# Optimization experiments

Measured on AMD Instinct MI355X. Metric: run time of the kernel, lower is better.

Reference implementation:

```python
import jax, jax.numpy as jnp
import numpy as np

B, L, H, E = 4, 2048, 8, 64  # S == L

def setup_inputs() -> dict:
    key = jax.random.key(0)
    k1, k2, k3, k4, k5 = jax.random.split(key, 5)
    q = jax.random.normal(k1, (B, L, H, E), dtype=jnp.float32)
    k = jax.random.normal(k2, (B, L, H, E), dtype=jnp.float32)
    v = jax.random.normal(k3, (B, L, H, E), dtype=jnp.float32)
    tau = jax.random.uniform(k4, (B, 1), dtype=jnp.float32) + 0.5  # positive scale
    delta = jax.random.normal(k5, (B, L), dtype=jnp.float32) * 0.1
    return {"q": q, "k": k, "v": v, "tau": tau, "delta": delta}

def reference(q, k, v, tau, delta):
    # De-stationarized attention: scores = (QK^T) * tau + delta, softmax(scale*scores)
    E_ = q.shape[-1]
    scale = 1.0 / jnp.sqrt(jnp.float32(E_))
    # tau: [B,1] -> [B,1,1,1]; delta: [B,S] -> [B,1,1,S]
    scores = jnp.einsum('blhe,bshe->bhls', q, k) * tau[:, None, None] + delta[:, None, None, :]
    a = jax.nn.softmax(scale * scores, axis=-1)  # dropout is identity in eval / p=0
    out = jnp.einsum('bhls,bshd->blhd', a, v)
    return out, a
```

## Files before the change

kernel.cpp:

```cpp
#include <hip/hip_runtime.h>
#include <stdint.h>

#define B_ 4
#define L_ 2048
#define H_ 8
#define E_ 64
#define S_ 2048

typedef __bf16 bf16x8 __attribute__((ext_vector_type(8)));
typedef _Float16 f16x8 __attribute__((ext_vector_type(8)));
typedef _Float16 f16x4 __attribute__((ext_vector_type(4)));
typedef float f32x4 __attribute__((ext_vector_type(4)));
typedef unsigned short u16;
typedef u16 u16x4 __attribute__((ext_vector_type(4)));

__device__ __forceinline__ u16 f32_to_bf16(float f) {
  union { float f; uint32_t u; } x;
  x.f = f;
  uint32_t u = x.u;
  return (u16)((u + 0x7FFFu + ((u >> 16) & 1u)) >> 16);
}

__global__ __launch_bounds__(256) void prep_qkd(
    const float* __restrict__ q, const float* __restrict__ k,
    const float* __restrict__ tau, const float* __restrict__ delta,
    u16* __restrict__ qb, u16* __restrict__ kb, float* __restrict__ dl) {
  int idx = blockIdx.x * 256 + threadIdx.x;
  int i4 = idx * 4;
  int b = i4 >> 20;
  const float C = 0.125f * 1.44269504088896f;
  float ts = tau[b] * C;
  f32x4 qv = *(const f32x4*)(q + i4);
  f32x4 kv = *(const f32x4*)(k + i4);
  u16x4 qs, ks;
#pragma unroll
  for (int j = 0; j < 4; ++j) {
    qs[j] = f32_to_bf16(qv[j] * ts);
    ks[j] = f32_to_bf16(kv[j]);
  }
  *(u16x4*)(qb + i4) = qs;
  *(u16x4*)(kb + i4) = ks;
  if (idx < (B_ * S_) / 4) {
    f32x4 dv = *(const f32x4*)(delta + i4);
    f32x4 ds = {dv[0] * C, dv[1] * C, dv[2] * C, dv[3] * C};
    *(f32x4*)(dl + i4) = ds;
  }
}

__global__ __launch_bounds__(256) void prep_v(const float* __restrict__ v,
                                              u16* __restrict__ vb) {
  __shared__ float t[32][33];
  int bid = blockIdx.x;
  int et = bid & 1;
  int st = (bid >> 1) & 63;
  int h = (bid >> 7) & 7;
  int b = bid >> 10;
  int tx = threadIdx.x & 31;
  int ty = threadIdx.x >> 5;
#pragma unroll
  for (int k2 = 0; k2 < 4; ++k2) {
    int s = st * 32 + ty + 8 * k2;
    int e = et * 32 + tx;
    t[ty + 8 * k2][tx] = v[(((size_t)b * S_ + s) * H_ + h) * E_ + e];
  }
  __syncthreads();
#pragma unroll
  for (int k2 = 0; k2 < 4; ++k2) {
    int e = et * 32 + ty + 8 * k2;
    int s = st * 32 + tx;
    _Float16 hf = (_Float16)t[tx][ty + 8 * k2];
    vb[(((size_t)b * H_ + h) * E_ + e) * S_ + s] = __builtin_bit_cast(u16, hf);
  }
}

__global__ __launch_bounds__(512, 4) void attn_fused(
    const u16* __restrict__ qb, const u16* __restrict__ kb,
    const u16* __restrict__ vbuf, const float* __restrict__ dl,
    float* __restrict__ out, float* __restrict__ oa) {
  __shared__ __align__(16) u16 sc[16 * 2048];
  __shared__ float psum[8][16];
  __shared__ float ox[4][16][17];

  int bid = blockIdx.x;
  int swz = (bid & 7) * 512 + (bid >> 3);
  int b = swz >> 10;
  int h = (swz >> 7) & 7;
  int qt = swz & 127;
  int m0 = qt * 16;
  int tid = threadIdx.x, lane = tid & 63, wave = tid >> 6;
  int l15 = lane & 15, l4 = lane >> 4;
  int s0 = wave * 256;
  int xm = (l15 & 7) << 4;
  char* scb = (char*)sc;

  const u16* qp = qb + (((size_t)b * L_ + (m0 + l15)) * H_ + h) * E_ + 8 * l4;
  bf16x8 qa0 = *(const bf16x8*)qp;
  bf16x8 qa1 = *(const bf16x8*)(qp + 32);

  const u16* kbase = kb + (((size_t)b * S_ + (s0 + l15)) * H_ + h) * E_ + 8 * l4;
  const float* dbase = dl + b * S_ + s0 + 4 * l4;

  float sums = 0.f;
#pragma unroll 4
  for (int t = 0; t < 16; ++t) {
    const u16* kp = kbase + (size_t)t * (16 * H_ * E_);
    bf16x8 ka0 = *(const bf16x8*)kp;
    bf16x8 ka1 = *(const bf16x8*)(kp + 32);
    f32x4 dv = *(const f32x4*)(dbase + 16 * t);
    f32x4 acc = {0.f, 0.f, 0.f, 0.f};
    acc = __builtin_amdgcn_mfma_f32_16x16x32_bf16(ka0, qa0, acc, 0, 0, 0);
    acc = __builtin_amdgcn_mfma_f32_16x16x32_bf16(ka1, qa1, acc, 0, 0, 0);
    float p0 = __builtin_amdgcn_exp2f(acc[0] + dv[0]);
    float p1 = __builtin_amdgcn_exp2f(acc[1] + dv[1]);
    float p2 = __builtin_amdgcn_exp2f(acc[2] + dv[2]);
    float p3 = __builtin_amdgcn_exp2f(acc[3] + dv[3]);
    sums += (p0 + p1) + (p2 + p3);
    f16x4 pv = {(_Float16)p0, (_Float16)p1, (_Float16)p2, (_Float16)p3};
    int off = (l15 << 12) + (((s0 << 1) + (t << 5) + (l4 << 3)) ^ xm);
    *(f16x4*)(scb + off) = pv;
  }
  sums += __shfl_xor(sums, 16, 64);
  sums += __shfl_xor(sums, 32, 64);
  if (lane < 16) psum[wave][lane] = sums;
  __syncthreads();

  float zq[2];

  {
    int et = wave & 3;
    int h2 = wave >> 2;
    const u16* vb0 =
        vbuf + ((size_t)(b * H_ + h) * E_ + 16 * et + l15) * S_ + h2 * 1024 + 8 * l4;
    const char* sch = scb + (l15 << 12) + (h2 << 11);
    f32x4 oaccA = {0.f, 0.f, 0.f, 0.f};
    f32x4 oaccB = {0.f, 0.f, 0.f, 0.f};
#pragma unroll 4
    for (int c = 0; c < 32; c += 2) {
      f16x8 af0 = *(const f16x8*)(sch + (((c << 6) + (l4 << 4)) ^ xm));
      f16x8 vf0 = *(const f16x8*)(vb0 + (c << 5));
      oaccA = __builtin_amdgcn_mfma_f32_16x16x32_f16(af0, vf0, oaccA, 0, 0, 0);
      f16x8 af1 = *(const f16x8*)(sch + ((((c + 1) << 6) + (l4 << 4)) ^ xm));
      f16x8 vf1 = *(const f16x8*)(vb0 + ((c + 1) << 5));
      oaccB = __builtin_amdgcn_mfma_f32_16x16x32_f16(af1, vf1, oaccB, 0, 0, 0);
    }
    oaccA += oaccB;
    if (h2 == 1) {
#pragma unroll
      for (int r = 0; r < 4; ++r) ox[et][4 * l4 + r][l15] = oaccA[r];
    }
    __syncthreads();
    if (h2 == 0) {
#pragma unroll
      for (int r = 0; r < 4; ++r) {
        int row = 4 * l4 + r;
        float zr = psum[0][row] + psum[1][row] + psum[2][row] + psum[3][row] +
                   psum[4][row] + psum[5][row] + psum[6][row] + psum[7][row];
        float o = oaccA[r] + ox[et][row][l15];
        out[(((size_t)b * L_ + (m0 + row)) * H_ + h) * E_ + 16 * et + l15] =
            o / zr;
      }
    }
  }

  {
    int row = 2 * wave + (lane >> 5);
    int l31 = lane & 31;
    float zrow = psum[0][row] + psum[1][row] + psum[2][row] + psum[3][row] +
                 psum[4][row] + psum[5][row] + psum[6][row] + psum[7][row];
    float zi = 1.f / zrow;
    float* ar = oa + (((size_t)(b * H_ + h)) * L_ + (m0 + row)) * S_;
    int xr = (row & 7) << 4;
    const char* scr = scb + (row << 12);
#pragma unroll 4
    for (int it = 0; it < 8; ++it) {
      f16x8 pv = *(const f16x8*)(scr + (((it << 9) + (l31 << 4)) ^ xr));
      f32x4 lo = {(float)pv[0] * zi, (float)pv[1] * zi,
                  (float)pv[2] * zi, (float)pv[3] * zi};
      f32x4 hi = {(float)pv[4] * zi, (float)pv[5] * zi,
                  (float)pv[6] * zi, (float)pv[7] * zi};
      int col = it * 256 + l31 * 8;
      *(f32x4*)(ar + col) = lo;
      *(f32x4*)(ar + col + 4) = hi;
    }
  }
}

extern "C" void kernel_launch(void* const* d_in, const int* in_sizes, int n_in,
                              void* d_out, int out_size, void* d_ws, size_t ws_size,
                              hipStream_t stream) {
  (void)in_sizes; (void)n_in; (void)out_size;
  const float* q = (const float*)d_in[0];
  const float* k = (const float*)d_in[1];
  const float* v = (const float*)d_in[2];
  const float* tau = (const float*)d_in[3];
  const float* delta = (const float*)d_in[4];
  float* out = (float*)d_out;
  float* oa = out + (size_t)B_ * L_ * H_ * E_;

  const size_t NQ = (size_t)B_ * L_ * H_ * E_;
  u16* qb = (u16*)d_ws;
  u16* kb = qb + NQ;
  u16* vb = kb + NQ;
  float* dl = (float*)(vb + NQ);
  size_t need = 3 * NQ * sizeof(u16) + (size_t)B_ * S_ * sizeof(float);
  if (ws_size < need) return;

  prep_qkd<<<4096, 256, 0, stream>>>(q, k, tau, delta, qb, kb, dl);
  prep_v<<<4096, 256, 0, stream>>>(v, vb);
  attn_fused<<<4096, 512, 0, stream>>>(qb, kb, vb, dl, out, oa);
}
```

Measured before the change: 341.9 us.

## Specialize waves: four compute PV while four stream normalized attention matrix

Splits the eight waves into two roles after the softmax stage. Waves 0-3 compute the P·V product, each doing two MFMAs per shared A fragment across 32 output columns. Waves 4-7 at the same time write the normalized fp32 attention matrix to global memory. This overlaps the large attention-matrix store with the PV compute instead of running them one after the other. The cost is fewer waves issuing stores and an extra barrier before the final output reduction.

```diff
diff --git a/kernel.cpp b/kernel.cpp
--- a/kernel.cpp
+++ b/kernel.cpp
@@ -79,7 +79,7 @@
     float* __restrict__ out, float* __restrict__ oa) {
   __shared__ __align__(16) u16 sc[16 * 2048];
   __shared__ float psum[8][16];
-  __shared__ float ox[4][16][17];
+  __shared__ float ox[2][16][33];
 
   int bid = blockIdx.x;
   int swz = (bid & 7) * 512 + (bid >> 3);
@@ -124,63 +124,66 @@
   if (lane < 16) psum[wave][lane] = sums;
   __syncthreads();
 
-  float zq[2];
-
-  {
-    int et = wave & 3;
-    int h2 = wave >> 2;
-    const u16* vb0 =
-        vbuf + ((size_t)(b * H_ + h) * E_ + 16 * et + l15) * S_ + h2 * 1024 + 8 * l4;
-    const char* sch = scb + (l15 << 12) + (h2 << 11);
-    f32x4 oaccA = {0.f, 0.f, 0.f, 0.f};
-    f32x4 oaccB = {0.f, 0.f, 0.f, 0.f};
+  f32x4 o0 = {0.f, 0.f, 0.f, 0.f};
+  f32x4 o1 = {0.f, 0.f, 0.f, 0.f};
+  int eh = wave & 1;
+
+  if (wave < 4) {
+    int sh = wave >> 1;
+    const u16* vb0 = vbuf + ((size_t)(b * H_ + h) * E_ + 32 * eh + l15) * S_ +
+                     sh * 1024 + 8 * l4;
+    const char* sch = scb + (l15 << 12) + (sh << 11);
 #pragma unroll 4
-    for (int c = 0; c < 32; c += 2) {
-      f16x8 af0 = *(const f16x8*)(sch + (((c << 6) + (l4 << 4)) ^ xm));
-      f16x8 vf0 = *(const f16x8*)(vb0 + (c << 5));
-      oaccA = __builtin_amdgcn_mfma_f32_16x16x32_f16(af0, vf0, oaccA, 0, 0, 0);
-      f16x8 af1 = *(const f16x8*)(sch + ((((c + 1) << 6) + (l4 << 4)) ^ xm));
-      f16x8 vf1 = *(const f16x8*)(vb0 + ((c + 1) << 5));
-      oaccB = __builtin_amdgcn_mfma_f32_16x16x32_f16(af1, vf1, oaccB, 0, 0, 0);
-    }
-    oaccA += oaccB;
-    if (h2 == 1) {
-#pragma unroll
-      for (int r = 0; r < 4; ++r) ox[et][4 * l4 + r][l15] = oaccA[r];
-    }
-    __syncthreads();
-    if (h2 == 0) {
+    for (int c = 0; c < 32; ++c) {
+      f16x8 af = *(const f16x8*)(sch + (((c << 6) + (l4 << 4)) ^ xm));
+      f16x8 v0 = *(const f16x8*)(vb0 + (c << 5));
+      f16x8 v1 = *(const f16x8*)(vb0 + 16 * S_ + (c << 5));
+      o0 = __builtin_amdgcn_mfma_f32_16x16x32_f16(af, v0, o0, 0, 0, 0);
+      o1 = __builtin_amdgcn_mfma_f32_16x16x32_f16(af, v1, o1, 0, 0, 0);
+    }
+    if (sh == 1) {
 #pragma unroll
       for (int r = 0; r < 4; ++r) {
-        int row = 4 * l4 + r;
-        float zr = psum[0][row] + psum[1][row] + psum[2][row] + psum[3][row] +
+        ox[eh][4 * l4 + r][l15] = o0[r];
+        ox[eh][4 * l4 + r][16 + l15] = o1[r];
+      }
+    }
+  } else {
+    int w4 = wave - 4;
+#pragma unroll
+    for (int rr = 0; rr < 4; ++rr) {
+      int row = w4 * 4 + rr;
+      float zrow = psum[0][row] + psum[1][row] + psum[2][row] + psum[3][row] +
                    psum[4][row] + psum[5][row] + psum[6][row] + psum[7][row];
-        float o = oaccA[r] + ox[et][row][l15];
-        out[(((size_t)b * L_ + (m0 + row)) * H_ + h) * E_ + 16 * et + l15] =
-            o / zr;
+      float zi = 1.f / zrow;
+      float* ar = oa + (((size_t)(b * H_ + h)) * L_ + (m0 + row)) * S_;
+      int xr = (row & 7) << 4;
+      const char* scr = scb + (row << 12);
+#pragma unroll
+      for (int it = 0; it < 4; ++it) {
+        f16x8 pv = *(const f16x8*)(scr + (((it << 10) + (lane << 4)) ^ xr));
+        f32x4 lo = {(float)pv[0] * zi, (float)pv[1] * zi,
+                    (float)pv[2] * zi, (float)pv[3] * zi};
+        f32x4 hi = {(float)pv[4] * zi, (float)pv[5] * zi,
+                    (float)pv[6] * zi, (float)pv[7] * zi};
+        int col = it * 512 + lane * 8;
+        *(f32x4*)(ar + col) = lo;
+        *(f32x4*)(ar + col + 4) = hi;
       }
     }
   }
-
-  {
-    int row = 2 * wave + (lane >> 5);
-    int l31 = lane & 31;
-    float zrow = psum[0][row] + psum[1][row] + psum[2][row] + psum[3][row] +
-                 psum[4][row] + psum[5][row] + psum[6][row] + psum[7][row];
-    float zi = 1.f / zrow;
-    float* ar = oa + (((size_t)(b * H_ + h)) * L_ + (m0 + row)) * S_;
-    int xr = (row & 7) << 4;
-    const char* scr = scb + (row << 12);
-#pragma unroll 4
-    for (int it = 0; it < 8; ++it) {
-      f16x8 pv = *(const f16x8*)(scr + (((it << 9) + (l31 << 4)) ^ xr));
-      f32x4 lo = {(float)pv[0] * zi, (float)pv[1] * zi,
-                  (float)pv[2] * zi, (float)pv[3] * zi};
-      f32x4 hi = {(float)pv[4] * zi, (float)pv[5] * zi,
-                  (float)pv[6] * zi, (float)pv[7] * zi};
-      int col = it * 256 + l31 * 8;
-      *(f32x4*)(ar + col) = lo;
-      *(f32x4*)(ar + col + 4) = hi;
+  __syncthreads();
+
+  if (wave < 2) {
+#pragma unroll
+    for (int r = 0; r < 4; ++r) {
+      int row = 4 * l4 + r;
+      float zrow = psum[0][row] + psum[1][row] + psum[2][row] + psum[3][row] +
+                   psum[4][row] + psum[5][row] + psum[6][row] + psum[7][row];
+      float zi = 1.f / zrow;
+      size_t ob = (((size_t)b * L_ + (m0 + row)) * H_ + h) * E_ + 32 * eh;
+      out[ob + l15] = (o0[r] + ox[eh][row][l15]) * zi;
+      out[ob + 16 + l15] = (o1[r] + ox[eh][row][16 + l15]) * zi;
     }
   }
 }
```

New measurement: 343.6 us. About the same (+0.5%).

## Split attention into compute kernel writing fp16 probabilities plus streaming normalize kernel

Applied to the files above, without the earlier changes.

When the workspace is large enough, the fused kernel is split in two. The first writes unnormalized fp16 probabilities and per-row inverse sums to the workspace. A second streaming kernel reads these back, normalizes them and writes the fp32 attention matrix with nontemporal stores. The aim is to decouple the compute-heavy phase from the large fp32 write, but it adds a full extra fp16 write and read of the attention matrix (about 256 MB of traffic). The original fused kernel is kept as a fallback when the workspace is too small.

```diff
diff --git a/kernel.cpp b/kernel.cpp
--- a/kernel.cpp
+++ b/kernel.cpp
@@ -73,10 +73,11 @@
   }
 }
 
-__global__ __launch_bounds__(512, 4) void attn_fused(
+__global__ __launch_bounds__(512, 4) void attn_compute(
     const u16* __restrict__ qb, const u16* __restrict__ kb,
     const u16* __restrict__ vbuf, const float* __restrict__ dl,
-    float* __restrict__ out, float* __restrict__ oa) {
+    float* __restrict__ out, u16* __restrict__ pbuf,
+    float* __restrict__ zinv_g) {
   __shared__ __align__(16) u16 sc[16 * 2048];
   __shared__ float psum[8][16];
   __shared__ float ox[4][16][17];
@@ -85,6 +86,7 @@
   int swz = (bid & 7) * 512 + (bid >> 3);
   int b = swz >> 10;
   int h = (swz >> 7) & 7;
+  int pane = (b << 3) | h;
   int qt = swz & 127;
   int m0 = qt * 16;
   int tid = threadIdx.x, lane = tid & 63, wave = tid >> 6;
@@ -124,13 +126,18 @@
   if (lane < 16) psum[wave][lane] = sums;
   __syncthreads();
 
-  float zq[2];
+  if (wave == 0 && lane < 16) {
+    int row = lane;
+    float zrow = psum[0][row] + psum[1][row] + psum[2][row] + psum[3][row] +
+                 psum[4][row] + psum[5][row] + psum[6][row] + psum[7][row];
+    zinv_g[((size_t)pane << 11) + m0 + row] = 1.f / zrow;
+  }
 
   {
     int et = wave & 3;
     int h2 = wave >> 2;
     const u16* vb0 =
-        vbuf + ((size_t)(b * H_ + h) * E_ + 16 * et + l15) * S_ + h2 * 1024 + 8 * l4;
+        vbuf + ((size_t)pane * E_ + 16 * et + l15) * S_ + h2 * 1024 + 8 * l4;
     const char* sch = scb + (l15 << 12) + (h2 << 11);
     f32x4 oaccA = {0.f, 0.f, 0.f, 0.f};
     f32x4 oaccB = {0.f, 0.f, 0.f, 0.f};
@@ -165,10 +172,125 @@
   {
     int row = 2 * wave + (lane >> 5);
     int l31 = lane & 31;
+    u16* pr = pbuf + (((size_t)pane << 11) + (m0 + row)) * S_;
+    int xr = (row & 7) << 4;
+    const char* scr = scb + (row << 12);
+#pragma unroll 4
+    for (int it = 0; it < 8; ++it) {
+      f16x8 pv = *(const f16x8*)(scr + (((it << 9) + (l31 << 4)) ^ xr));
+      __builtin_nontemporal_store(pv, (f16x8*)(pr + it * 256 + l31 * 8));
+    }
+  }
+}
+
+__global__ __launch_bounds__(256) void finalize_a(
+    const u16* __restrict__ pbuf, const float* __restrict__ zinv_g,
+    float* __restrict__ oa) {
+  size_t idx = (size_t)blockIdx.x * 256 + threadIdx.x;
+  size_t row = idx >> 8;
+  float zi = zinv_g[row];
+  f16x8 pv = __builtin_nontemporal_load((const f16x8*)(pbuf + idx * 8));
+  f32x4 lo = {(float)pv[0] * zi, (float)pv[1] * zi, (float)pv[2] * zi,
+              (float)pv[3] * zi};
+  f32x4 hi = {(float)pv[4] * zi, (float)pv[5] * zi, (float)pv[6] * zi,
+              (float)pv[7] * zi};
+  float* o = oa + idx * 8;
+  __builtin_nontemporal_store(lo, (f32x4*)o);
+  __builtin_nontemporal_store(hi, (f32x4*)(o + 4));
+}
+
+__global__ __launch_bounds__(512, 4) void attn_fused(
+    const u16* __restrict__ qb, const u16* __restrict__ kb,
+    const u16* __restrict__ vbuf, const float* __restrict__ dl,
+    float* __restrict__ out, float* __restrict__ oa) {
+  __shared__ __align__(16) u16 sc[16 * 2048];
+  __shared__ float psum[8][16];
+  __shared__ float ox[4][16][17];
+
+  int bid = blockIdx.x;
+  int swz = (bid & 7) * 512 + (bid >> 3);
+  int b = swz >> 10;
+  int h = (swz >> 7) & 7;
+  int qt = swz & 127;
+  int m0 = qt * 16;
+  int tid = threadIdx.x, lane = tid & 63, wave = tid >> 6;
+  int l15 = lane & 15, l4 = lane >> 4;
+  int s0 = wave * 256;
+  int xm = (l15 & 7) << 4;
+  char* scb = (char*)sc;
+
+  const u16* qp = qb + (((size_t)b * L_ + (m0 + l15)) * H_ + h) * E_ + 8 * l4;
+  bf16x8 qa0 = *(const bf16x8*)qp;
+  bf16x8 qa1 = *(const bf16x8*)(qp + 32);
+  const u16* kbase = kb + (((size_t)b * S_ + (s0 + l15)) * H_ + h) * E_ + 8 * l4;
+  const float* dbase = dl + b * S_ + s0 + 4 * l4;
+
+  float sums = 0.f;
+#pragma unroll 4
+  for (int t = 0; t < 16; ++t) {
+    const u16* kp = kbase + (size_t)t * (16 * H_ * E_);
+    bf16x8 ka0 = *(const bf16x8*)kp;
+    bf16x8 ka1 = *(const bf16x8*)(kp + 32);
+    f32x4 dv = *(const f32x4*)(dbase + 16 * t);
+    f32x4 acc = {0.f, 0.f, 0.f, 0.f};
+    acc = __builtin_amdgcn_mfma_f32_16x16x32_bf16(ka0, qa0, acc, 0, 0, 0);
+    acc = __builtin_amdgcn_mfma_f32_16x16x32_bf16(ka1, qa1, acc, 0, 0, 0);
+    float p0 = __builtin_amdgcn_exp2f(acc[0] + dv[0]);
+    float p1 = __builtin_amdgcn_exp2f(acc[1] + dv[1]);
+    float p2 = __builtin_amdgcn_exp2f(acc[2] + dv[2]);
+    float p3 = __builtin_amdgcn_exp2f(acc[3] + dv[3]);
+    sums += (p0 + p1) + (p2 + p3);
+    f16x4 pv = {(_Float16)p0, (_Float16)p1, (_Float16)p2, (_Float16)p3};
+    int off = (l15 << 12) + (((s0 << 1) + (t << 5) + (l4 << 3)) ^ xm);
+    *(f16x4*)(scb + off) = pv;
+  }
+  sums += __shfl_xor(sums, 16, 64);
+  sums += __shfl_xor(sums, 32, 64);
+  if (lane < 16) psum[wave][lane] = sums;
+  __syncthreads();
+
+  {
+    int et = wave & 3;
+    int h2 = wave >> 2;
+    const u16* vb0 =
+        vbuf + ((size_t)((b << 3) | h) * E_ + 16 * et + l15) * S_ + h2 * 1024 + 8 * l4;
+    const char* sch = scb + (l15 << 12) + (h2 << 11);
+    f32x4 oaccA = {0.f, 0.f, 0.f, 0.f};
+    f32x4 oaccB = {0.f, 0.f, 0.f, 0.f};
+#pragma unroll 4
+    for (int c = 0; c < 32; c += 2) {
+      f16x8 af0 = *(const f16x8*)(sch + (((c << 6) + (l4 << 4)) ^ xm));
+      f16x8 vf0 = *(const f16x8*)(vb0 + (c << 5));
+      oaccA = __builtin_amdgcn_mfma_f32_16x16x32_f16(af0, vf0, oaccA, 0, 0, 0);
+      f16x8 af1 = *(const f16x8*)(sch + ((((c + 1) << 6) + (l4 << 4)) ^ xm));
+      f16x8 vf1 = *(const f16x8*)(vb0 + ((c + 1) << 5));
+      oaccB = __builtin_amdgcn_mfma_f32_16x16x32_f16(af1, vf1, oaccB, 0, 0, 0);
+    }
+    oaccA += oaccB;
+    if (h2 == 1) {
+#pragma unroll
+      for (int r = 0; r < 4; ++r) ox[et][4 * l4 + r][l15] = oaccA[r];
+    }
+    __syncthreads();
+    if (h2 == 0) {
+#pragma unroll
+      for (int r = 0; r < 4; ++r) {
+        int row = 4 * l4 + r;
+        float zr = psum[0][row] + psum[1][row] + psum[2][row] + psum[3][row] +
+                   psum[4][row] + psum[5][row] + psum[6][row] + psum[7][row];
+        float o = oaccA[r] + ox[et][row][l15];
+        out[(((size_t)b * L_ + (m0 + row)) * H_ + h) * E_ + 16 * et + l15] =
+            o / zr;
+      }
+    }
+  }
+  {
+    int row = 2 * wave + (lane >> 5);
+    int l31 = lane & 31;
     float zrow = psum[0][row] + psum[1][row] + psum[2][row] + psum[3][row] +
                  psum[4][row] + psum[5][row] + psum[6][row] + psum[7][row];
     float zi = 1.f / zrow;
-    float* ar = oa + (((size_t)(b * H_ + h)) * L_ + (m0 + row)) * S_;
+    float* ar = oa + (((size_t)((b << 3) | h)) * L_ + (m0 + row)) * S_;
     int xr = (row & 7) << 4;
     const char* scr = scb + (row << 12);
 #pragma unroll 4
@@ -198,14 +320,24 @@
   float* oa = out + (size_t)B_ * L_ * H_ * E_;
 
   const size_t NQ = (size_t)B_ * L_ * H_ * E_;
+  const size_t NA = (size_t)B_ * H_ * L_ * S_;
   u16* qb = (u16*)d_ws;
   u16* kb = qb + NQ;
   u16* vb = kb + NQ;
   float* dl = (float*)(vb + NQ);
-  size_t need = 3 * NQ * sizeof(u16) + (size_t)B_ * S_ * sizeof(float);
-  if (ws_size < need) return;
+  float* zinv_g = dl + (size_t)B_ * S_;
+  u16* pbuf = (u16*)(zinv_g + (size_t)B_ * H_ * L_);
+  size_t need_small = 3 * NQ * sizeof(u16) + (size_t)B_ * S_ * sizeof(float);
+  size_t need_split = need_small + (size_t)B_ * H_ * L_ * sizeof(float) +
+                      NA * sizeof(u16);
+  if (ws_size < need_small) return;
 
   prep_qkd<<<4096, 256, 0, stream>>>(q, k, tau, delta, qb, kb, dl);
   prep_v<<<4096, 256, 0, stream>>>(v, vb);
-  attn_fused<<<4096, 512, 0, stream>>>(qb, kb, vb, dl, out, oa);
-}
+  if (ws_size >= need_split) {
+    attn_compute<<<4096, 512, 0, stream>>>(qb, kb, vb, dl, out, pbuf, zinv_g);
+    finalize_a<<<(int)(NA / 8 / 256), 256, 0, stream>>>(pbuf, zinv_g, oa);
+  } else {
+    attn_fused<<<4096, 512, 0, stream>>>(qb, kb, vb, dl, out, oa);
+  }
+}
```

New measurement: 495.3 us. +44.9%, slower.
